# Kernel tuning notes

Measured on AMD Instinct MI355X. Metric: run time of the kernel, lower is better.

Reference implementation:

```python
import jax, jax.numpy as jnp
import numpy as np

B, L, E, V = 4, 4096, 512, 256
BLOCKS = 4
BLOCK_SIZES = [2, 3, 4]  # block width per grouping layer
PAD = 0


def setup_inputs() -> dict:
    key = jax.random.key(0)
    k1, k2, k3, k4 = jax.random.split(key, 4)
    # character ids in [1, V) so no position is padding (mask stays all-False)
    sequence = jax.random.randint(k1, (B, L), 1, V, dtype=jnp.int32)
    # contiguous, sorted, 1-based group ids; identical across batch (so the
    # torch code's shared repeat_interleave counts are exact)
    pos = jnp.arange(L, dtype=jnp.int32)
    gids = jnp.stack([pos // bs + 1 for bs in BLOCK_SIZES])  # [BLOCKS-1, L]
    group_id = jnp.broadcast_to(gids[None], (B, BLOCKS - 1, L)).astype(jnp.int32)
    emb = jax.random.normal(k2, (V, E), jnp.float32) * 0.02
    emb = emb.at[PAD].set(0.0)  # padding_idx row
    score_w = jax.random.normal(k3, (E,), jnp.float32) * 0.02
    score_b = jax.random.normal(k4, (1,), jnp.float32) * 0.02
    return {"sequence": sequence, "group_id": group_id, "emb": emb,
            "score_w": score_w, "score_b": score_b}


def _segment_mean(x, seg, num_segments):
    # x: [L, E], seg: [L] -> [num_segments, E]
    s = jax.ops.segment_sum(x, seg, num_segments=num_segments)
    c = jax.ops.segment_sum(jnp.ones((x.shape[0],), x.dtype), seg,
                            num_segments=num_segments)
    return jnp.where(c[:, None] > 0, s / jnp.maximum(c, 1.0)[:, None], 0.0)


def reference(sequence, group_id, emb, score_w, score_b):
    Bx, Lx = sequence.shape
    embed = emb[sequence]                                   # [B, L, E]
    blocks_mask = jnp.concatenate([sequence[:, None, :], group_id], axis=1)  # [B, K, L]
    max_gid = group_id.max(axis=2)                          # [B, K-1]
    embed_det = jax.lax.stop_gradient(embed)                # torch .detach()
    num_seg = Lx + 1  # safe upper bound on number of groups
    reps = [embed]
    for layer in range(group_id.shape[1]):
        gid = group_id[:, layer]                            # [B, L]
        blocked = jax.vmap(lambda xb, gb: _segment_mean(xb, gb, num_seg))(
            embed_det, gid)                                 # [B, L+1, E]
        # torch scatter_mean + bincount(gid-1) + repeat_interleave collapses
        # (for contiguous sorted groups) to gathering blocked[gid'-1], where
        # gid' replaces pad positions with max_gid+1 (off-by-one preserved).
        idx = jnp.where(gid == PAD, max_gid[:, layer:layer + 1] + 1, gid) - 1
        reps.append(jnp.take_along_axis(blocked, idx[:, :, None], axis=1))
    block_reps = jnp.stack(reps, axis=2)                    # [B, L, K, E]
    scores = jnp.einsum('blke,e->blk', block_reps, score_w) + score_b[0]
    mask = jnp.transpose(blocks_mask, (0, 2, 1)) == PAD     # [B, L, K]
    neg = -jnp.finfo(scores.dtype).max
    weights = jax.nn.softmax(jnp.where(mask, neg, scores), axis=2)
    return jnp.sum(block_reps * weights[..., None], axis=2)  # [B, L, E]
```

## Files before the change

### kernel.cpp

```cpp
#include <hip/hip_runtime.h>

#define L_SEQ 4096
#define E_DIM 512
#define B_DIM 4

typedef float f32x4 __attribute__((ext_vector_type(4)));

__global__ __launch_bounds__(256) void k_fused(const int* __restrict__ seq,
                                               const float* __restrict__ emb,
                                               const float* __restrict__ w,
                                               float* __restrict__ out) {
    int wid = threadIdx.x >> 6;
    int lane = threadIdx.x & 63;
    int row = blockIdx.x * 4 + wid;
    int b = row >> 12;
    int l = row & (L_SEQ - 1);
    const int* seqb = seq + b * L_SEQ;

    int j2 = (l >> 1) - 1, j3 = l / 3 - 1, j4 = (l >> 2) - 1;
    int s2 = j2 * 2, s3 = j3 * 3, s4 = j4 * 4;
    int lo = max(min(min(s2, s3), min(s4, l)), 0);

    const f32x4* w4 = (const f32x4*)w;
    f32x4 wv0 = w4[lane];
    f32x4 wv1 = w4[lane + 64];

    f32x4 e0[8], e1[8];
#pragma unroll
    for (int i = 0; i < 8; ++i) {
        int p = lo + i;
        int v = seqb[min(p, l)];
        const f32x4* er = (const f32x4*)(emb + v * E_DIM);
        e0[i] = er[lane];
        e1[i] = er[lane + 64];
    }

    float t0 = 0.f, t1 = 0.f, t2 = 0.f, t3 = 0.f;
#pragma unroll
    for (int i = 0; i < 8; ++i) {
        int p = lo + i;
        f32x4 d4 = e0[i] * wv0 + e1[i] * wv1;
        float d = d4.x + d4.y + d4.z + d4.w;
        if (p == l) t0 += d;
        if ((unsigned)(p - s2) < 2u) t1 += d;
        if ((unsigned)(p - s3) < 3u) t2 += d;
        if ((unsigned)(p - s4) < 4u) t3 += d;
    }
#pragma unroll
    for (int off = 32; off > 0; off >>= 1) {
        t0 += __shfl_xor(t0, off);
        t1 += __shfl_xor(t1, off);
        t2 += __shfl_xor(t2, off);
        t3 += __shfl_xor(t3, off);
    }
    float sc0 = t0;
    float sc1 = t1 * 0.5f;
    float sc2 = t2 * (1.f / 3.f);
    float sc3 = t3 * 0.25f;

    float m = fmaxf(fmaxf(sc0, sc1), fmaxf(sc2, sc3));
    float q0 = __expf(sc0 - m), q1 = __expf(sc1 - m);
    float q2 = __expf(sc2 - m), q3 = __expf(sc3 - m);
    float inv = 1.f / (q0 + q1 + q2 + q3);
    float c0 = q0 * inv;
    float c1 = q1 * inv * 0.5f;
    float c2 = q2 * inv * (1.f / 3.f);
    float c3 = q3 * inv * 0.25f;

    f32x4 a0 = {0.f, 0.f, 0.f, 0.f};
    f32x4 a1 = {0.f, 0.f, 0.f, 0.f};
#pragma unroll
    for (int i = 0; i < 8; ++i) {
        int p = lo + i;
        float cc = (p == l) ? c0 : 0.f;
        if ((unsigned)(p - s2) < 2u) cc += c1;
        if ((unsigned)(p - s3) < 3u) cc += c2;
        if ((unsigned)(p - s4) < 4u) cc += c3;
        a0 += cc * e0[i];
        a1 += cc * e1[i];
    }

    f32x4* orow = (f32x4*)(out + (size_t)row * E_DIM);
    __builtin_nontemporal_store(a0, &orow[lane]);
    __builtin_nontemporal_store(a1, &orow[lane + 64]);
}

extern "C" void kernel_launch(void* const* d_in, const int* in_sizes, int n_in,
                              void* d_out, int out_size, void* d_ws, size_t ws_size,
                              hipStream_t stream) {
    const int* seq = (const int*)d_in[0];
    const float* emb = (const float*)d_in[2];
    const float* sw = (const float*)d_in[3];
    float* out = (float*)d_out;

    const int n = B_DIM * L_SEQ;
    k_fused<<<n / 4, 256, 0, stream>>>(seq, emb, sw, out);
}
```

Baseline: 82.85 us.

## Process two adjacent output rows per wavefront sharing one embedding window

Each wavefront now computes two consecutive sequence positions, loading a single 8-row embedding window (l0-6..l0+1) and reusing it for both rows' group-mean scores and weighted sums. Out-of-range window rows are zeroed with a multiply instead of clamping the window start. This halves the number of wavefronts and the embedding gathers per output row, at the cost of more registers per thread and fewer waves in flight.

```diff
diff --git a/kernel.cpp b/kernel.cpp
--- a/kernel.cpp
+++ b/kernel.cpp
@@ -6,20 +6,21 @@
 
 typedef float f32x4 __attribute__((ext_vector_type(4)));
 
-__global__ __launch_bounds__(256) void k_fused(const int* __restrict__ seq,
-                                               const float* __restrict__ emb,
-                                               const float* __restrict__ w,
-                                               float* __restrict__ out) {
+__global__ __launch_bounds__(256) void k_fused2(const int* __restrict__ seq,
+                                                const float* __restrict__ emb,
+                                                const float* __restrict__ w,
+                                                float* __restrict__ out) {
     int wid = threadIdx.x >> 6;
     int lane = threadIdx.x & 63;
-    int row = blockIdx.x * 4 + wid;
-    int b = row >> 12;
-    int l = row & (L_SEQ - 1);
+    int q = blockIdx.x * 4 + wid;
+    int b = q >> 11;
+    int l0 = (q & 2047) * 2;
+    int l1 = l0 + 1;
     const int* seqb = seq + b * L_SEQ;
 
-    int j2 = (l >> 1) - 1, j3 = l / 3 - 1, j4 = (l >> 2) - 1;
-    int s2 = j2 * 2, s3 = j3 * 3, s4 = j4 * 4;
-    int lo = max(min(min(s2, s3), min(s4, l)), 0);
+    int s2a = ((l0 >> 1) - 1) * 2, s3a = (l0 / 3 - 1) * 3, s4a = ((l0 >> 2) - 1) * 4;
+    int s2b = ((l1 >> 1) - 1) * 2, s3b = (l1 / 3 - 1) * 3, s4b = ((l1 >> 2) - 1) * 4;
+    int W = l0 - 6;
 
     const f32x4* w4 = (const f32x4*)w;
     f32x4 wv0 = w4[lane];
@@ -28,61 +29,78 @@
     f32x4 e0[8], e1[8];
 #pragma unroll
     for (int i = 0; i < 8; ++i) {
-        int p = lo + i;
-        int v = seqb[min(p, l)];
+        int p = W + i;
+        int v = seqb[max(p, 0)];
         const f32x4* er = (const f32x4*)(emb + v * E_DIM);
-        e0[i] = er[lane];
-        e1[i] = er[lane + 64];
+        float keep = (p >= 0) ? 1.f : 0.f;
+        e0[i] = er[lane] * keep;
+        e1[i] = er[lane + 64] * keep;
     }
 
-    float t0 = 0.f, t1 = 0.f, t2 = 0.f, t3 = 0.f;
+    float tA0 = 0.f, tA1 = 0.f, tA2 = 0.f, tA3 = 0.f;
+    float tB0 = 0.f, tB1 = 0.f, tB2 = 0.f, tB3 = 0.f;
 #pragma unroll
     for (int i = 0; i < 8; ++i) {
-        int p = lo + i;
+        int p = W + i;
         f32x4 d4 = e0[i] * wv0 + e1[i] * wv1;
         float d = d4.x + d4.y + d4.z + d4.w;
-        if (p == l) t0 += d;
-        if ((unsigned)(p - s2) < 2u) t1 += d;
-        if ((unsigned)(p - s3) < 3u) t2 += d;
-        if ((unsigned)(p - s4) < 4u) t3 += d;
+        if (p == l0) tA0 += d;
+        if ((unsigned)(p - s2a) < 2u) tA1 += d;
+        if ((unsigned)(p - s3a) < 3u) tA2 += d;
+        if ((unsigned)(p - s4a) < 4u) tA3 += d;
+        if (p == l1) tB0 += d;
+        if ((unsigned)(p - s2b) < 2u) tB1 += d;
+        if ((unsigned)(p - s3b) < 3u) tB2 += d;
+        if ((unsigned)(p - s4b) < 4u) tB3 += d;
     }
 #pragma unroll
     for (int off = 32; off > 0; off >>= 1) {
-        t0 += __shfl_xor(t0, off);
-        t1 += __shfl_xor(t1, off);
-        t2 += __shfl_xor(t2, off);
-        t3 += __shfl_xor(t3, off);
+        tA0 += __shfl_xor(tA0, off); tA1 += __shfl_xor(tA1, off);
+        tA2 += __shfl_xor(tA2, off); tA3 += __shfl_xor(tA3, off);
+        tB0 += __shfl_xor(tB0, off); tB1 += __shfl_xor(tB1, off);
+        tB2 += __shfl_xor(tB2, off); tB3 += __shfl_xor(tB3, off);
     }
-    float sc0 = t0;
-    float sc1 = t1 * 0.5f;
-    float sc2 = t2 * (1.f / 3.f);
-    float sc3 = t3 * 0.25f;
 
-    float m = fmaxf(fmaxf(sc0, sc1), fmaxf(sc2, sc3));
-    float q0 = __expf(sc0 - m), q1 = __expf(sc1 - m);
-    float q2 = __expf(sc2 - m), q3 = __expf(sc3 - m);
-    float inv = 1.f / (q0 + q1 + q2 + q3);
-    float c0 = q0 * inv;
-    float c1 = q1 * inv * 0.5f;
-    float c2 = q2 * inv * (1.f / 3.f);
-    float c3 = q3 * inv * 0.25f;
+    float scA1 = tA1 * 0.5f, scA2 = tA2 * (1.f / 3.f), scA3 = tA3 * 0.25f;
+    float mA = fmaxf(fmaxf(tA0, scA1), fmaxf(scA2, scA3));
+    float qA0 = __expf(tA0 - mA), qA1 = __expf(scA1 - mA);
+    float qA2 = __expf(scA2 - mA), qA3 = __expf(scA3 - mA);
+    float invA = 1.f / (qA0 + qA1 + qA2 + qA3);
+    float cA0 = qA0 * invA, cA1 = qA1 * invA * 0.5f;
+    float cA2 = qA2 * invA * (1.f / 3.f), cA3 = qA3 * invA * 0.25f;
 
-    f32x4 a0 = {0.f, 0.f, 0.f, 0.f};
-    f32x4 a1 = {0.f, 0.f, 0.f, 0.f};
+    float scB1 = tB1 * 0.5f, scB2 = tB2 * (1.f / 3.f), scB3 = tB3 * 0.25f;
+    float mB = fmaxf(fmaxf(tB0, scB1), fmaxf(scB2, scB3));
+    float qB0 = __expf(tB0 - mB), qB1 = __expf(scB1 - mB);
+    float qB2 = __expf(scB2 - mB), qB3 = __expf(scB3 - mB);
+    float invB = 1.f / (qB0 + qB1 + qB2 + qB3);
+    float cB0 = qB0 * invB, cB1 = qB1 * invB * 0.5f;
+    float cB2 = qB2 * invB * (1.f / 3.f), cB3 = qB3 * invB * 0.25f;
+
+    f32x4 aA0 = {0.f, 0.f, 0.f, 0.f}, aA1 = {0.f, 0.f, 0.f, 0.f};
+    f32x4 aB0 = {0.f, 0.f, 0.f, 0.f}, aB1 = {0.f, 0.f, 0.f, 0.f};
 #pragma unroll
     for (int i = 0; i < 8; ++i) {
-        int p = lo + i;
-        float cc = (p == l) ? c0 : 0.f;
-        if ((unsigned)(p - s2) < 2u) cc += c1;
-        if ((unsigned)(p - s3) < 3u) cc += c2;
-        if ((unsigned)(p - s4) < 4u) cc += c3;
-        a0 += cc * e0[i];
-        a1 += cc * e1[i];
+        int p = W + i;
+        float ca = (p == l0) ? cA0 : 0.f;
+        if ((unsigned)(p - s2a) < 2u) ca += cA1;
+        if ((unsigned)(p - s3a) < 3u) ca += cA2;
+        if ((unsigned)(p - s4a) < 4u) ca += cA3;
+        float cb = (p == l1) ? cB0 : 0.f;
+        if ((unsigned)(p - s2b) < 2u) cb += cB1;
+        if ((unsigned)(p - s3b) < 3u) cb += cB2;
+        if ((unsigned)(p - s4b) < 4u) cb += cB3;
+        aA0 += ca * e0[i]; aA1 += ca * e1[i];
+        aB0 += cb * e0[i]; aB1 += cb * e1[i];
     }
 
-    f32x4* orow = (f32x4*)(out + (size_t)row * E_DIM);
-    __builtin_nontemporal_store(a0, &orow[lane]);
-    __builtin_nontemporal_store(a1, &orow[lane + 64]);
+    size_t base = (size_t)(b * L_SEQ + l0) * E_DIM;
+    f32x4* rowA = (f32x4*)(out + base);
+    f32x4* rowB = (f32x4*)(out + base + E_DIM);
+    __builtin_nontemporal_store(aA0, &rowA[lane]);
+    __builtin_nontemporal_store(aA1, &rowA[lane + 64]);
+    __builtin_nontemporal_store(aB0, &rowB[lane]);
+    __builtin_nontemporal_store(aB1, &rowB[lane + 64]);
 }
 
 extern "C" void kernel_launch(void* const* d_in, const int* in_sizes, int n_in,
@@ -93,6 +111,6 @@
     const float* sw = (const float*)d_in[3];
     float* out = (float*)d_out;
 
-    const int n = B_DIM * L_SEQ;
-    k_fused<<<n / 4, 256, 0, stream>>>(seq, emb, sw, out);
+    const int npairs = B_DIM * L_SEQ / 2;
+    k_fused2<<<npairs / 4, 256, 0, stream>>>(seq, emb, sw, out);
 }
```

New measurement: 77.49 us. 6.5% less time.
